# Kernel optimization log

Hardware: AMD Instinct MI355X
Metric: run time of the kernel (lower is better)

The kernel has to match this reference:

```python
import jax, jax.numpy as jnp
import numpy as np

D_MODEL = 512
N_HEADS = 8
D_KV = 64
EPS = 1e-6
ROPE_THETA = 10000.0


def _rms_norm(x, w):
    # T5-style RMSNorm: no mean subtraction, no bias, variance in fp32.
    var = jnp.mean(x.astype(jnp.float32) ** 2, axis=-1, keepdims=True)
    return (x * jax.lax.rsqrt(var + EPS)).astype(x.dtype) * w


def _rope_cos_sin(pos, dk):
    # pos: [B, T] int -> cos/sin: [B, 1, T, dk]
    inv_freq = 1.0 / (ROPE_THETA ** (jnp.arange(0, dk, 2, dtype=jnp.float32) / dk))
    ang = pos.astype(jnp.float32)[:, :, None] * inv_freq[None, None, :]  # [B,T,dk/2]
    ang = jnp.concatenate([ang, ang], axis=-1)                            # [B,T,dk]
    return jnp.cos(ang)[:, None], jnp.sin(ang)[:, None]


def _rotate_half(x):
    h = x.shape[-1] // 2
    return jnp.concatenate([-x[..., h:], x[..., :h]], axis=-1)


def _mha(x, mask, wq, wk, wv, wo, pos=None):
    # x: [B, T, D]; mask: [B, H, T, T] additive
    B, T, _ = x.shape
    def proj(w):
        return (x @ w).reshape(B, T, N_HEADS, D_KV).transpose(0, 2, 1, 3)  # [B,H,T,dk]
    q, k, v = proj(wq), proj(wk), proj(wv)
    if pos is not None:
        cos, sin = _rope_cos_sin(pos, D_KV)
        cos, sin = cos.astype(x.dtype), sin.astype(x.dtype)
        q = q * cos + _rotate_half(q) * sin
        k = k * cos + _rotate_half(k) * sin
    scale = 1.0 / np.sqrt(D_KV)
    scores = jnp.einsum('bhqd,bhkd->bhqk', q, k) * scale + mask
    attn = jax.nn.softmax(scores.astype(jnp.float32), axis=-1).astype(scores.dtype)
    out = jnp.einsum('bhqk,bhkd->bhqd', attn, v)
    out = out.transpose(0, 2, 1, 3).reshape(B, T, N_HEADS * D_KV)
    return out @ wo


def setup_inputs() -> dict:
    key = jax.random.key(0)
    ks = jax.random.split(key, 12)
    B, T = 8, 1024
    s = 1.0 / np.sqrt(D_MODEL)
    inp = {
        'h': jax.random.normal(ks[0], (B, T, D_MODEL), dtype=jnp.float32),
        'pos': jnp.broadcast_to(jnp.arange(T, dtype=jnp.int64 if jax.config.jax_enable_x64 else jnp.int32)[None, :], (B, T)),
        't_mask': jnp.zeros((B, N_HEADS, T, T), dtype=jnp.float32),
        'g_mask': jnp.zeros((T, N_HEADS, B, B), dtype=jnp.float32),
        'ln_t_w': jnp.ones((D_MODEL,), dtype=jnp.float32),
        'ln_g_w': jnp.ones((D_MODEL,), dtype=jnp.float32),
    }
    names = ['wq_t', 'wk_t', 'wv_t', 'wo_t', 'wq_g', 'wk_g', 'wv_g', 'wo_g']
    for i, n in enumerate(names):
        inp[n] = jax.random.normal(ks[i + 1], (D_MODEL, D_MODEL), dtype=jnp.float32) * s
    return inp


def reference(h, pos, t_mask, g_mask, ln_t_w, ln_g_w,
              wq_t, wk_t, wv_t, wo_t, wq_g, wk_g, wv_g, wo_g):
    # --- time attention (over T axis, with RoPE) ---
    normed = _rms_norm(h, ln_t_w)
    attn_t = _mha(normed, t_mask, wq_t, wk_t, wv_t, wo_t, pos=pos)
    h = h + attn_t  # dropout p=0 (eval)
    # --- group attention (over B axis, no RoPE) ---
    h = h.transpose(1, 0, 2)  # [T, B, D]
    normed = _rms_norm(h, ln_g_w)
    attn_g = _mha(normed, g_mask, wq_g, wk_g, wv_g, wo_g, pos=None)
    h = h + attn_g
    return h.transpose(1, 0, 2)  # back to [B, T, D]
```

## Files before the change

### kernel.cpp

```cpp
#include <hip/hip_runtime.h>
#include <hip/hip_bf16.h>
#include <math.h>


typedef __bf16 bf16x8 __attribute__((ext_vector_type(8)));
typedef __bf16 bf16x4 __attribute__((ext_vector_type(4)));
typedef float  f32x4  __attribute__((ext_vector_type(4)));

#define LN1E4_OVER_32 0.2878231366242558f

__device__ __forceinline__ void gld16(const void* g, void* l) {
    __builtin_amdgcn_global_load_lds((const __attribute__((address_space(1))) void*)g,
                                     (__attribute__((address_space(3))) void*)l,
                                     16, 0, 0);
}

__global__ __launch_bounds__(256) void transpose_w(
    const float* w0, const float* w1, const float* w2, const float* w3,
    const float* w4, const float* w5, const float* w6, const float* w7,
    __bf16* qkvT_t, __bf16* oT_t, __bf16* qkvT_g, __bf16* oT_g)
{
    int mat = blockIdx.z;
    const float* src; __bf16* dst; int rowOff;
    switch (mat) {
        case 0: src=w0; dst=qkvT_t; rowOff=0;    break;
        case 1: src=w1; dst=qkvT_t; rowOff=512;  break;
        case 2: src=w2; dst=qkvT_t; rowOff=1024; break;
        case 3: src=w3; dst=oT_t;   rowOff=0;    break;
        case 4: src=w4; dst=qkvT_g; rowOff=0;    break;
        case 5: src=w5; dst=qkvT_g; rowOff=512;  break;
        case 6: src=w6; dst=qkvT_g; rowOff=1024; break;
        default: src=w7; dst=oT_g;  rowOff=0;    break;
    }
    __shared__ float tile[32][33];
    int n0 = blockIdx.x * 32, k0 = blockIdx.y * 32;
    int tt = threadIdx.x;
    int kr = tt >> 3, nc = (tt & 7) * 4;
    float4 v = *(const float4*)(src + (size_t)(k0 + kr) * 512 + n0 + nc);
    tile[kr][nc+0] = v.x; tile[kr][nc+1] = v.y; tile[kr][nc+2] = v.z; tile[kr][nc+3] = v.w;
    __syncthreads();
    int nr = tt >> 3, kc = (tt & 7) * 4;
    bf16x4 o;
    o[0] = (__bf16)tile[kc+0][nr]; o[1] = (__bf16)tile[kc+1][nr];
    o[2] = (__bf16)tile[kc+2][nr]; o[3] = (__bf16)tile[kc+3][nr];
    *(bf16x4*)(dst + (size_t)(rowOff + n0 + nr) * 512 + k0 + kc) = o;
}

__global__ __launch_bounds__(256) void rmsnorm_k(
    const float* __restrict__ x, const float* __restrict__ w,
    __bf16* __restrict__ y, int remap)
{
    int row = blockIdx.x * 4 + (threadIdx.x >> 6);
    int l = threadIdx.x & 63;
    const float* xr = x + (size_t)row * 512 + l * 8;
    float4 a = *(const float4*)xr;
    float4 b = *(const float4*)(xr + 4);
    float ss = a.x*a.x + a.y*a.y + a.z*a.z + a.w*a.w
             + b.x*b.x + b.y*b.y + b.z*b.z + b.w*b.w;
    for (int m = 1; m < 64; m <<= 1) ss += __shfl_xor(ss, m);
    float rms = rsqrtf(ss * (1.0f / 512.0f) + 1e-6f);
    float4 wa = *(const float4*)(w + l * 8);
    float4 wb = *(const float4*)(w + l * 8 + 4);
    int orow = remap ? ((row & 1023) * 8 + (row >> 10)) : row;
    bf16x8 o;
    o[0] = (__bf16)(a.x * rms * wa.x); o[1] = (__bf16)(a.y * rms * wa.y);
    o[2] = (__bf16)(a.z * rms * wa.z); o[3] = (__bf16)(a.w * rms * wa.w);
    o[4] = (__bf16)(b.x * rms * wb.x); o[5] = (__bf16)(b.y * rms * wb.y);
    o[6] = (__bf16)(b.z * rms * wb.z); o[7] = (__bf16)(b.w * rms * wb.w);
    *(bf16x8*)(y + (size_t)orow * 512 + l * 8) = o;
}

__global__ __launch_bounds__(256) void gemm_ep(
    const __bf16* __restrict__ A, const __bf16* __restrict__ Bt,
    const int* __restrict__ pos, const float* __restrict__ resid,
    float* __restrict__ outF,
    __bf16* __restrict__ o0, __bf16* __restrict__ o1, __bf16* __restrict__ o2,
    int mode)
{
    __shared__ __bf16 smem[8192];
    __bf16* As = smem;
    __bf16* Bs = smem + 4096;
    int tid = threadIdx.x;
    int l = tid & 63, w = tid >> 6;
    int l16 = l & 15, quad = l >> 4;
    int wm = w >> 1, wn = w & 1;
    int mblk = blockIdx.y * 128, nblk = blockIdx.x * 128;
    f32x4 acc[4][4] = {};

    for (int k0 = 0; k0 < 512; k0 += 32) {
        __syncthreads();
        #pragma unroll
        for (int i = 0; i < 2; ++i) {
            int idx = i * 256 + tid;
            int row = idx >> 2, c8 = (idx & 3) * 8;
            gld16(A  + (size_t)(mblk + row) * 512 + k0 + c8, (char*)As + (size_t)idx * 16);
            gld16(Bt + (size_t)(nblk + row) * 512 + k0 + c8, (char*)Bs + (size_t)idx * 16);
        }
        __syncthreads();
        bf16x8 aF[4], bF[4];
        #pragma unroll
        for (int mt = 0; mt < 4; mt++) aF[mt] = *(bf16x8*)(As + (wm * 64 + mt * 16 + l16) * 32 + quad * 8);
        #pragma unroll
        for (int nt = 0; nt < 4; nt++) bF[nt] = *(bf16x8*)(Bs + (wn * 64 + nt * 16 + l16) * 32 + quad * 8);
        #pragma unroll
        for (int mt = 0; mt < 4; mt++)
            #pragma unroll
            for (int nt = 0; nt < 4; nt++)
                acc[mt][nt] = __builtin_amdgcn_mfma_f32_16x16x32_bf16(aF[mt], bF[nt], acc[mt][nt], 0, 0, 0);
    }
    __syncthreads();

    int colbase = nblk + wn * 64;
    if (mode == 0 || mode == 2) {
        int mat = colbase >> 9;
        int hh  = (colbase & 511) >> 6;
        __bf16* dst = (mat == 0) ? o0 : (mat == 1) ? o1 : o2;
        bool isQ = (mat == 0), isV = (mat == 2);
        if (mode == 0 && isV) {
            __bf16* vls = smem + (size_t)w * 1536;
            #pragma unroll
            for (int mt = 0; mt < 4; mt++) {
                #pragma unroll
                for (int nt = 0; nt < 4; nt++)
                    #pragma unroll
                    for (int r = 0; r < 4; r++)
                        vls[(nt * 16 + l16) * 24 + quad * 4 + r] = (__bf16)acc[mt][nt][r];
                int grow0 = mblk + wm * 64 + mt * 16;
                int b = grow0 >> 10, t0 = grow0 & 1023;
                #pragma unroll
                for (int i = 0; i < 2; ++i) {
                    int li = i * 64 + l;
                    int d = li >> 1, t8 = (li & 1) * 8;
                    bf16x8 vv = *(bf16x8*)&vls[d * 24 + t8];
                    *(bf16x8*)&dst[((size_t)(b * 8 + hh) * 64 + d) * 1024 + t0 + t8] = vv;
                }
            }
        } else {
            #pragma unroll
            for (int mt = 0; mt < 4; mt++) {
                #pragma unroll
                for (int r = 0; r < 4; r++) {
                    int grow = mblk + wm * 64 + mt * 16 + quad * 4 + r;
                    if (mode == 0) {
                        int b = grow >> 10, t = grow & 1023;
                        int p = pos[grow];
                        #pragma unroll
                        for (int nt = 0; nt < 2; nt++) {
                            int i = nt * 16 + l16;
                            float ang = (float)p * __expf((float)i * -LN1E4_OVER_32);
                            float c, s; __sincosf(ang, &s, &c);
                            float x1 = acc[mt][nt][r], x2 = acc[mt][nt + 2][r];
                            float y1 = x1 * c - x2 * s;
                            float y2 = x2 * c + x1 * s;
                            if (isQ) { y1 *= 0.125f; y2 *= 0.125f; }
                            size_t base = ((size_t)(b * 8 + hh) * 1024 + t) * 64;
                            dst[base + i]      = (__bf16)y1;
                            dst[base + i + 32] = (__bf16)y2;
                        }
                    } else {
                        int t = grow >> 3, b = grow & 7;
                        size_t base = (((size_t)t * 8 + hh) * 8 + b) * 64;
                        #pragma unroll
                        for (int nt = 0; nt < 4; nt++) {
                            float v = acc[mt][nt][r];
                            if (isQ) v *= 0.125f;
                            dst[base + nt * 16 + l16] = (__bf16)v;
                        }
                    }
                }
            }
        }
    } else {
        #pragma unroll
        for (int mt = 0; mt < 4; mt++)
            #pragma unroll
            for (int r = 0; r < 4; r++) {
                int grow = mblk + wm * 64 + mt * 16 + quad * 4 + r;
                int orow = (mode == 3) ? (((grow & 7) << 10) + (grow >> 3)) : grow;
                #pragma unroll
                for (int nt = 0; nt < 4; nt++) {
                    int col = colbase + nt * 16 + l16;
                    size_t oi = (size_t)orow * 512 + col;
                    outF[oi] = acc[mt][nt][r] + resid[oi];
                }
            }
    }
}

__global__ __launch_bounds__(256) void flash_t(
    const __bf16* __restrict__ q, const __bf16* __restrict__ k,
    const __bf16* __restrict__ vt, const float* __restrict__ tmask,
    __bf16* __restrict__ ctx)
{
    int bh = blockIdx.y;
    int w = threadIdx.x >> 6, l = threadIdx.x & 63;
    int l16 = l & 15, quad = l >> 4;
    int q0 = blockIdx.x * 64 + w * 16;

    __shared__ __bf16 Ks[64 * 72];
    __shared__ __bf16 Vs[64 * 72];
    __shared__ __bf16 Ps[4][16 * 72];

    bf16x8 aQ0, aQ1;
    {
        const __bf16* qb = q + ((size_t)bh * 1024 + q0 + l16) * 64 + quad * 8;
        aQ0 = *(const bf16x8*)qb;
        aQ1 = *(const bf16x8*)(qb + 32);
    }
    f32x4 o[4] = {};
    float m_i[4], l_i[4];
    #pragma unroll
    for (int r = 0; r < 4; r++) { m_i[r] = -INFINITY; l_i[r] = 0.0f; }

    for (int jb = 0; jb < 1024; jb += 64) {
        __syncthreads();
        #pragma unroll
        for (int it = 0; it < 2; ++it) {
            int c = threadIdx.x + it * 256;
            int row = c >> 3, col = (c & 7) << 3;
            *(bf16x8*)&Ks[row * 72 + col] = *(const bf16x8*)&k [((size_t)bh * 1024 + jb + row) * 64 + col];
            *(bf16x8*)&Vs[row * 72 + col] = *(const bf16x8*)&vt[((size_t)bh * 64 + row) * 1024 + jb + col];
        }
        __syncthreads();

        f32x4 s[4] = {};
        #pragma unroll
        for (int nt = 0; nt < 4; nt++) {
            bf16x8 b0 = *(bf16x8*)&Ks[(nt * 16 + l16) * 72 + quad * 8];
            bf16x8 b1 = *(bf16x8*)&Ks[(nt * 16 + l16) * 72 + 32 + quad * 8];
            s[nt] = __builtin_amdgcn_mfma_f32_16x16x32_bf16(aQ0, b0, s[nt], 0, 0, 0);
            s[nt] = __builtin_amdgcn_mfma_f32_16x16x32_bf16(aQ1, b1, s[nt], 0, 0, 0);
        }
        const float* mr = tmask + (size_t)bh * 1024 * 1024 + (size_t)(q0 + quad * 4) * 1024 + jb + l16;
        #pragma unroll
        for (int r = 0; r < 4; r++)
            #pragma unroll
            for (int nt = 0; nt < 4; nt++)
                s[nt][r] += mr[(size_t)r * 1024 + nt * 16];

        float alpha[4];
        #pragma unroll
        for (int r = 0; r < 4; r++) {
            float mx = fmaxf(fmaxf(s[0][r], s[1][r]), fmaxf(s[2][r], s[3][r]));
            mx = fmaxf(mx, __shfl_xor(mx, 1));
            mx = fmaxf(mx, __shfl_xor(mx, 2));
            mx = fmaxf(mx, __shfl_xor(mx, 4));
            mx = fmaxf(mx, __shfl_xor(mx, 8));
            float mn = fmaxf(m_i[r], mx);
            alpha[r] = __expf(m_i[r] - mn);
            m_i[r] = mn;
            float rs = 0.0f;
            #pragma unroll
            for (int nt = 0; nt < 4; nt++) {
                float p = __expf(s[nt][r] - mn);
                s[nt][r] = p;
                rs += p;
            }
            rs += __shfl_xor(rs, 1);
            rs += __shfl_xor(rs, 2);
            rs += __shfl_xor(rs, 4);
            rs += __shfl_xor(rs, 8);
            l_i[r] = l_i[r] * alpha[r] + rs;
        }
        #pragma unroll
        for (int dt = 0; dt < 4; dt++)
            #pragma unroll
            for (int r = 0; r < 4; r++) o[dt][r] *= alpha[r];

        __bf16* ps = Ps[w];
        #pragma unroll
        for (int nt = 0; nt < 4; nt++)
            #pragma unroll
            for (int r = 0; r < 4; r++)
                ps[(quad * 4 + r) * 72 + nt * 16 + l16] = (__bf16)s[nt][r];
        bf16x8 aP0 = *(bf16x8*)&ps[l16 * 72 + quad * 8];
        bf16x8 aP1 = *(bf16x8*)&ps[l16 * 72 + 32 + quad * 8];
        #pragma unroll
        for (int dt = 0; dt < 4; dt++) {
            bf16x8 bv0 = *(bf16x8*)&Vs[(dt * 16 + l16) * 72 + quad * 8];
            bf16x8 bv1 = *(bf16x8*)&Vs[(dt * 16 + l16) * 72 + 32 + quad * 8];
            o[dt] = __builtin_amdgcn_mfma_f32_16x16x32_bf16(aP0, bv0, o[dt], 0, 0, 0);
            o[dt] = __builtin_amdgcn_mfma_f32_16x16x32_bf16(aP1, bv1, o[dt], 0, 0, 0);
        }
    }

    int b = bh >> 3, h = bh & 7;
    #pragma unroll
    for (int dt = 0; dt < 4; dt++)
        #pragma unroll
        for (int r = 0; r < 4; r++) {
            float v = o[dt][r] / l_i[r];
            ctx[((size_t)b * 1024 + q0 + quad * 4 + r) * 512 + h * 64 + dt * 16 + l16] = (__bf16)v;
        }
}

__global__ __launch_bounds__(256) void group_attn(
    const __bf16* __restrict__ qg, const __bf16* __restrict__ kg,
    const __bf16* __restrict__ vg, const float* __restrict__ gmask,
    __bf16* __restrict__ ctxg)
{
    int tid = blockIdx.x * 256 + threadIdx.x;
    int t = tid >> 6, h = (tid >> 3) & 7, bq = tid & 7;
    size_t base = ((size_t)t * 8 + h) * 512;

    float qv[64];
    #pragma unroll
    for (int d0 = 0; d0 < 64; d0 += 8) {
        bf16x8 qq = *(const bf16x8*)&qg[base + (size_t)bq * 64 + d0];
        #pragma unroll
        for (int u = 0; u < 8; u++) qv[d0 + u] = (float)qq[u];
    }
    float s[8];
    #pragma unroll
    for (int j = 0; j < 8; j++) {
        float acc = 0.0f;
        #pragma unroll
        for (int d0 = 0; d0 < 64; d0 += 8) {
            bf16x8 kk = *(const bf16x8*)&kg[base + (size_t)j * 64 + d0];
            #pragma unroll
            for (int u = 0; u < 8; u++) acc += qv[d0 + u] * (float)kk[u];
        }
        s[j] = acc + gmask[(((size_t)t * 8 + h) * 8 + bq) * 8 + j];
    }
    float mx = s[0];
    #pragma unroll
    for (int j = 1; j < 8; j++) mx = fmaxf(mx, s[j]);
    float sum = 0.0f;
    #pragma unroll
    for (int j = 0; j < 8; j++) { s[j] = __expf(s[j] - mx); sum += s[j]; }
    float inv = 1.0f / sum;

    #pragma unroll
    for (int d0 = 0; d0 < 64; d0 += 8) {
        float o8[8] = {};
        #pragma unroll
        for (int j = 0; j < 8; j++) {
            bf16x8 vv = *(const bf16x8*)&vg[base + (size_t)j * 64 + d0];
            float pj = s[j];
            #pragma unroll
            for (int u = 0; u < 8; u++) o8[u] += pj * (float)vv[u];
        }
        bf16x8 ob;
        #pragma unroll
        for (int u = 0; u < 8; u++) ob[u] = (__bf16)(o8[u] * inv);
        *(bf16x8*)&ctxg[((size_t)t * 8 + bq) * 512 + h * 64 + d0] = ob;
    }
}

extern "C" void kernel_launch(void* const* d_in, const int* in_sizes, int n_in,
                              void* d_out, int out_size, void* d_ws, size_t ws_size,
                              hipStream_t stream)
{
    const float* h      = (const float*)d_in[0];
    const int*   pos    = (const int*)  d_in[1];
    const float* t_mask = (const float*)d_in[2];
    const float* g_mask = (const float*)d_in[3];
    const float* ln_t_w = (const float*)d_in[4];
    const float* ln_g_w = (const float*)d_in[5];
    const float* wq_t = (const float*)d_in[6];
    const float* wk_t = (const float*)d_in[7];
    const float* wv_t = (const float*)d_in[8];
    const float* wo_t = (const float*)d_in[9];
    const float* wq_g = (const float*)d_in[10];
    const float* wk_g = (const float*)d_in[11];
    const float* wv_g = (const float*)d_in[12];
    const float* wo_g = (const float*)d_in[13];
    float* out = (float*)d_out;

    char* ws = (char*)d_ws;
    const size_t MB = 1ull << 20;
    __bf16* qkvT_t = (__bf16*)ws;
    __bf16* oT_t   = qkvT_t + 786432;
    __bf16* qkvT_g = qkvT_t + 1048576;
    __bf16* oT_g   = qkvT_t + 1835008;
    __bf16* normed = (__bf16*)(ws + 4 * MB);
    __bf16* qb     = (__bf16*)(ws + 12 * MB);
    __bf16* kb     = (__bf16*)(ws + 20 * MB);
    __bf16* vb     = (__bf16*)(ws + 28 * MB);
    __bf16* ctx    = (__bf16*)(ws + 36 * MB);
    float*  h2     = (float*) (ws + 44 * MB);

    transpose_w<<<dim3(16, 16, 8), 256, 0, stream>>>(
        wq_t, wk_t, wv_t, wo_t, wq_g, wk_g, wv_g, wo_g,
        qkvT_t, oT_t, qkvT_g, oT_g);

    rmsnorm_k<<<2048, 256, 0, stream>>>(h, ln_t_w, normed, 0);
    gemm_ep<<<dim3(12, 64), 256, 0, stream>>>(normed, qkvT_t, pos, nullptr, nullptr,
                                              qb, kb, vb, 0);
    flash_t<<<dim3(16, 64), 256, 0, stream>>>(qb, kb, vb, t_mask, ctx);
    gemm_ep<<<dim3(4, 64), 256, 0, stream>>>(ctx, oT_t, nullptr, h, h2,
                                             nullptr, nullptr, nullptr, 1);

    rmsnorm_k<<<2048, 256, 0, stream>>>(h2, ln_g_w, normed, 1);
    gemm_ep<<<dim3(12, 64), 256, 0, stream>>>(normed, qkvT_g, nullptr, nullptr, nullptr,
                                              qb, kb, vb, 2);
    group_attn<<<256, 256, 0, stream>>>(qb, kb, vb, g_mask, ctx);
    gemm_ep<<<dim3(4, 64), 256, 0, stream>>>(ctx, oT_g, nullptr, h2, out,
                                             nullptr, nullptr, nullptr, 3);
}
```

Before: 542.2 us.

## Stage GEMM epilogues and flash mask loads through LDS for coalesced access

The GEMM epilogues now write accumulator tiles into per-wave LDS scratch and then emit 16-byte vectorized global stores, replacing scattered 2-byte bf16 and 4-byte float stores. The residual-add path also reads and writes float4. The RoPE frequencies are hoisted per lane and positions are loaded as int4. In flash_t, the 64x64 fp32 mask tile is brought into LDS with async global_load_lds, replacing strided per-lane global reads, and the ctx output is written through LDS as bf16x8. This adds 16KB of LDS to flash_t, which may reduce occupancy, and adds extra LDS round trips.

```diff
diff --git a/kernel.cpp b/kernel.cpp
--- a/kernel.cpp
+++ b/kernel.cpp
@@ -77,9 +77,9 @@
     __bf16* __restrict__ o0, __bf16* __restrict__ o1, __bf16* __restrict__ o2,
     int mode)
 {
-    __shared__ __bf16 smem[8192];
-    __bf16* As = smem;
-    __bf16* Bs = smem + 4096;
+    __shared__ float fsm[4][1088];
+    __bf16* As = (__bf16*)fsm;
+    __bf16* Bs = As + 4096;
     int tid = threadIdx.x;
     int l = tid & 63, w = tid >> 6;
     int l16 = l & 15, quad = l >> 4;
@@ -111,79 +111,109 @@
     __syncthreads();
 
     int colbase = nblk + wn * 64;
+    __bf16* bw = ((__bf16*)fsm) + w * 1536;
+    float*  fw = (float*)((char*)fsm + w * 4352);
+    int rbrow = l >> 3, rbch = (l & 7) * 8;
+
     if (mode == 0 || mode == 2) {
         int mat = colbase >> 9;
         int hh  = (colbase & 511) >> 6;
         __bf16* dst = (mat == 0) ? o0 : (mat == 1) ? o1 : o2;
         bool isQ = (mat == 0), isV = (mat == 2);
-        if (mode == 0 && isV) {
-            __bf16* vls = smem + (size_t)w * 1536;
+        if (mode == 0 && !isV) {
+            float f0 = __expf((float)l16        * -LN1E4_OVER_32);
+            float f1 = __expf((float)(16 + l16) * -LN1E4_OVER_32);
+            #pragma unroll
+            for (int mt = 0; mt < 4; mt++) {
+                int grow0 = mblk + wm * 64 + mt * 16;
+                int b = grow0 >> 10, t0 = grow0 & 1023;
+                int4 p4 = *(const int4*)&pos[grow0 + quad * 4];
+                const int pa[4] = {p4.x, p4.y, p4.z, p4.w};
+                #pragma unroll
+                for (int r = 0; r < 4; r++) {
+                    float p = (float)pa[r];
+                    #pragma unroll
+                    for (int nt = 0; nt < 2; nt++) {
+                        int i = nt * 16 + l16;
+                        float ang = p * (nt ? f1 : f0);
+                        float c, s; __sincosf(ang, &s, &c);
+                        float x1 = acc[mt][nt][r], x2 = acc[mt][nt + 2][r];
+                        float y1 = x1 * c - x2 * s;
+                        float y2 = x2 * c + x1 * s;
+                        if (isQ) { y1 *= 0.125f; y2 *= 0.125f; }
+                        bw[(quad * 4 + r) * 72 + i]      = (__bf16)y1;
+                        bw[(quad * 4 + r) * 72 + i + 32] = (__bf16)y2;
+                    }
+                }
+                #pragma unroll
+                for (int i = 0; i < 2; ++i) {
+                    int rr = rbrow + i * 8;
+                    bf16x8 vv = *(bf16x8*)&bw[rr * 72 + rbch];
+                    *(bf16x8*)&dst[((size_t)(b * 8 + hh) * 1024 + t0 + rr) * 64 + rbch] = vv;
+                }
+            }
+        } else if (mode == 0) {
             #pragma unroll
             for (int mt = 0; mt < 4; mt++) {
                 #pragma unroll
                 for (int nt = 0; nt < 4; nt++)
                     #pragma unroll
                     for (int r = 0; r < 4; r++)
-                        vls[(nt * 16 + l16) * 24 + quad * 4 + r] = (__bf16)acc[mt][nt][r];
+                        bw[(nt * 16 + l16) * 24 + quad * 4 + r] = (__bf16)acc[mt][nt][r];
                 int grow0 = mblk + wm * 64 + mt * 16;
                 int b = grow0 >> 10, t0 = grow0 & 1023;
                 #pragma unroll
                 for (int i = 0; i < 2; ++i) {
                     int li = i * 64 + l;
                     int d = li >> 1, t8 = (li & 1) * 8;
-                    bf16x8 vv = *(bf16x8*)&vls[d * 24 + t8];
+                    bf16x8 vv = *(bf16x8*)&bw[d * 24 + t8];
                     *(bf16x8*)&dst[((size_t)(b * 8 + hh) * 64 + d) * 1024 + t0 + t8] = vv;
                 }
             }
         } else {
             #pragma unroll
             for (int mt = 0; mt < 4; mt++) {
-                #pragma unroll
-                for (int r = 0; r < 4; r++) {
-                    int grow = mblk + wm * 64 + mt * 16 + quad * 4 + r;
-                    if (mode == 0) {
-                        int b = grow >> 10, t = grow & 1023;
-                        int p = pos[grow];
-                        #pragma unroll
-                        for (int nt = 0; nt < 2; nt++) {
-                            int i = nt * 16 + l16;
-                            float ang = (float)p * __expf((float)i * -LN1E4_OVER_32);
-                            float c, s; __sincosf(ang, &s, &c);
-                            float x1 = acc[mt][nt][r], x2 = acc[mt][nt + 2][r];
-                            float y1 = x1 * c - x2 * s;
-                            float y2 = x2 * c + x1 * s;
-                            if (isQ) { y1 *= 0.125f; y2 *= 0.125f; }
-                            size_t base = ((size_t)(b * 8 + hh) * 1024 + t) * 64;
-                            dst[base + i]      = (__bf16)y1;
-                            dst[base + i + 32] = (__bf16)y2;
-                        }
-                    } else {
-                        int t = grow >> 3, b = grow & 7;
-                        size_t base = (((size_t)t * 8 + hh) * 8 + b) * 64;
-                        #pragma unroll
-                        for (int nt = 0; nt < 4; nt++) {
-                            float v = acc[mt][nt][r];
-                            if (isQ) v *= 0.125f;
-                            dst[base + nt * 16 + l16] = (__bf16)v;
-                        }
+                int grow0 = mblk + wm * 64 + mt * 16;
+                #pragma unroll
+                for (int nt = 0; nt < 4; nt++)
+                    #pragma unroll
+                    for (int r = 0; r < 4; r++) {
+                        float v = acc[mt][nt][r];
+                        if (isQ) v *= 0.125f;
+                        bw[(quad * 4 + r) * 72 + nt * 16 + l16] = (__bf16)v;
                     }
+                #pragma unroll
+                for (int i = 0; i < 2; ++i) {
+                    int rr = rbrow + i * 8;
+                    int grow = grow0 + rr;
+                    int t = grow >> 3, bq = grow & 7;
+                    bf16x8 vv = *(bf16x8*)&bw[rr * 72 + rbch];
+                    *(bf16x8*)&dst[(((size_t)t * 8 + hh) * 8 + bq) * 64 + rbch] = vv;
                 }
             }
         }
     } else {
         #pragma unroll
-        for (int mt = 0; mt < 4; mt++)
-            #pragma unroll
-            for (int r = 0; r < 4; r++) {
-                int grow = mblk + wm * 64 + mt * 16 + quad * 4 + r;
+        for (int mt = 0; mt < 4; mt++) {
+            int grow0 = mblk + wm * 64 + mt * 16;
+            #pragma unroll
+            for (int nt = 0; nt < 4; nt++)
+                #pragma unroll
+                for (int r = 0; r < 4; r++)
+                    fw[(quad * 4 + r) * 68 + nt * 16 + l16] = acc[mt][nt][r];
+            #pragma unroll
+            for (int i = 0; i < 4; ++i) {
+                int rr = i * 4 + (l >> 4);
+                int c4 = (l & 15) * 4;
+                f32x4 a4 = *(f32x4*)&fw[rr * 68 + c4];
+                int grow = grow0 + rr;
                 int orow = (mode == 3) ? (((grow & 7) << 10) + (grow >> 3)) : grow;
-                #pragma unroll
-                for (int nt = 0; nt < 4; nt++) {
-                    int col = colbase + nt * 16 + l16;
-                    size_t oi = (size_t)orow * 512 + col;
-                    outF[oi] = acc[mt][nt][r] + resid[oi];
-                }
+                size_t oi = (size_t)orow * 512 + colbase + c4;
+                f32x4 r4 = *(const f32x4*)&resid[oi];
+                r4 += a4;
+                *(f32x4*)&outF[oi] = r4;
             }
+        }
     }
 }
 
@@ -195,22 +225,26 @@
     int bh = blockIdx.y;
     int w = threadIdx.x >> 6, l = threadIdx.x & 63;
     int l16 = l & 15, quad = l >> 4;
-    int q0 = blockIdx.x * 64 + w * 16;
+    int qb0 = blockIdx.x * 64;
+    int q0 = qb0 + w * 16;
 
     __shared__ __bf16 Ks[64 * 72];
     __shared__ __bf16 Vs[64 * 72];
     __shared__ __bf16 Ps[4][16 * 72];
+    __shared__ float  Ms[64 * 64];
 
     bf16x8 aQ0, aQ1;
     {
-        const __bf16* qb = q + ((size_t)bh * 1024 + q0 + l16) * 64 + quad * 8;
-        aQ0 = *(const bf16x8*)qb;
-        aQ1 = *(const bf16x8*)(qb + 32);
+        const __bf16* qp = q + ((size_t)bh * 1024 + q0 + l16) * 64 + quad * 8;
+        aQ0 = *(const bf16x8*)qp;
+        aQ1 = *(const bf16x8*)(qp + 32);
     }
     f32x4 o[4] = {};
     float m_i[4], l_i[4];
     #pragma unroll
     for (int r = 0; r < 4; r++) { m_i[r] = -INFINITY; l_i[r] = 0.0f; }
+
+    const float* mbase = tmask + (size_t)bh * 1024 * 1024;
 
     for (int jb = 0; jb < 1024; jb += 64) {
         __syncthreads();
@@ -221,6 +255,12 @@
             *(bf16x8*)&Ks[row * 72 + col] = *(const bf16x8*)&k [((size_t)bh * 1024 + jb + row) * 64 + col];
             *(bf16x8*)&Vs[row * 72 + col] = *(const bf16x8*)&vt[((size_t)bh * 64 + row) * 1024 + jb + col];
         }
+        #pragma unroll
+        for (int it = 0; it < 4; ++it) {
+            int c = it * 256 + threadIdx.x;
+            int row = c >> 4, ch = c & 15;
+            gld16(mbase + (size_t)(qb0 + row) * 1024 + jb + ch * 4, (char*)Ms + (size_t)c * 16);
+        }
         __syncthreads();
 
         f32x4 s[4] = {};
@@ -231,12 +271,11 @@
             s[nt] = __builtin_amdgcn_mfma_f32_16x16x32_bf16(aQ0, b0, s[nt], 0, 0, 0);
             s[nt] = __builtin_amdgcn_mfma_f32_16x16x32_bf16(aQ1, b1, s[nt], 0, 0, 0);
         }
-        const float* mr = tmask + (size_t)bh * 1024 * 1024 + (size_t)(q0 + quad * 4) * 1024 + jb + l16;
         #pragma unroll
         for (int r = 0; r < 4; r++)
             #pragma unroll
             for (int nt = 0; nt < 4; nt++)
-                s[nt][r] += mr[(size_t)r * 1024 + nt * 16];
+                s[nt][r] += Ms[(w * 16 + quad * 4 + r) * 64 + nt * 16 + l16];
 
         float alpha[4];
         #pragma unroll
@@ -285,13 +324,19 @@
     }
 
     int b = bh >> 3, h = bh & 7;
+    __bf16* ps = Ps[w];
     #pragma unroll
     for (int dt = 0; dt < 4; dt++)
         #pragma unroll
-        for (int r = 0; r < 4; r++) {
-            float v = o[dt][r] / l_i[r];
-            ctx[((size_t)b * 1024 + q0 + quad * 4 + r) * 512 + h * 64 + dt * 16 + l16] = (__bf16)v;
-        }
+        for (int r = 0; r < 4; r++)
+            ps[(quad * 4 + r) * 72 + dt * 16 + l16] = (__bf16)(o[dt][r] / l_i[r]);
+    int rbrow = l >> 3, rbch = (l & 7) * 8;
+    #pragma unroll
+    for (int i = 0; i < 2; ++i) {
+        int rr = rbrow + i * 8;
+        bf16x8 vv = *(bf16x8*)&ps[rr * 72 + rbch];
+        *(bf16x8*)&ctx[((size_t)b * 1024 + q0 + rr) * 512 + h * 64 + rbch] = vv;
+    }
 }
 
 __global__ __launch_bounds__(256) void group_attn(
```

New measurement: 569.8 us. +5.1%, slower.
